# Kernel tuning notes

Measured on AMD Instinct MI355X. Metric: run time of the kernel, lower is better.

Reference implementation:

```python
import jax, jax.numpy as jnp
import numpy as np

M, IN, OUT, R = 8192, 4096, 4096, 16  # tokens, in_features, out_features, lora rank


def setup_inputs() -> dict:
    key = jax.random.key(0)
    k = jax.random.split(key, 7)
    # symmetric int8 quantized activations and weights
    x = jax.random.randint(k[0], (M, IN), -127, 128, dtype=jnp.int8)
    weight = jax.random.randint(k[1], (OUT, IN), -127, 128, dtype=jnp.int8)
    # per-token activation scales and per-output-channel weight scales
    x_scales = jax.random.uniform(k[2], (M,), jnp.float32, 0.5, 1.5) / 127.0
    scales = jax.random.uniform(k[3], (OUT,), jnp.float32, 0.5, 1.5) / 127.0
    bias = jax.random.normal(k[4], (OUT,), jnp.float32)
    # module inits lora_a ~ N(0, 1/r); lora_b is zeros in the module but we use
    # small random values so the LoRA path is numerically exercised
    lora_a = jax.random.normal(k[5], (R, IN), jnp.float32) * (1.0 / R)
    lora_b = jax.random.normal(k[6], (OUT, R), jnp.float32) * 0.02
    return dict(x=x, weight=weight, bias=bias, x_scales=x_scales,
                scales=scales, lora_a=lora_a, lora_b=lora_b, fuse_gelu=1)


def reference(x, weight, bias, x_scales, scales, lora_a, lora_b, fuse_gelu):
    acc = jax.lax.dot_general(x, weight, (((1,), (1,)), ((), ())),
                              preferred_element_type=jnp.int32)
    # dequantize with outer product of per-token and per-channel scales
    main = acc.astype(jnp.float32) * x_scales[:, None] * scales[None, :]
    # LoRA correction on the dequantized activations: (x_deq @ A^T) @ B^T
    x_deq = x.astype(jnp.float32) * x_scales[:, None]          # [M, IN]
    lora = (x_deq @ lora_a.T) @ lora_b.T                        # [M, R] @ [R, OUT]
    out = main + lora + bias[None, :]
    if fuse_gelu:  # static Python flag
        out = jax.nn.gelu(out, approximate=True)  # tanh-approx GELU (CUDA fused path)
    return out
```

## Files before the change

### kernel.cpp

```cpp
#include <hip/hip_runtime.h>

#define M_DIM 8192
#define IN_DIM 4096
#define OUT_DIM 4096

typedef int   v4i  __attribute__((ext_vector_type(4)));
typedef int   v16i __attribute__((ext_vector_type(16)));
typedef short v8s  __attribute__((ext_vector_type(8)));
typedef float v4f  __attribute__((ext_vector_type(4)));
typedef float v16f __attribute__((ext_vector_type(16)));

static __device__ __forceinline__ int pack4(int a, int b, int c, int d) {
    return (a & 255) | ((b & 255) << 8) | ((c & 255) << 16) | ((d & 255) << 24);
}

static __device__ __forceinline__ short f2bf(float f) {
    unsigned u = __float_as_uint(f);
    u = (u + 0x7FFFu + ((u >> 16) & 1u)) >> 16;
    return (short)u;
}

static __device__ __forceinline__ short i2bf(int v) {
    float f = (float)v;
    return (short)(__float_as_uint(f) >> 16);
}

static __device__ __forceinline__ float gelu_tanh(float u) {
    float u2 = u * u;
    float p  = fmaf(u2, 0.0356774081f, 0.7978845608f);
    float v  = u * p;
    float e  = __builtin_amdgcn_exp2f(v * 2.8853900818f);
    return u - u * __builtin_amdgcn_rcpf(e + 1.0f);
}

static __device__ __forceinline__ void async_cp16(const signed char* g, signed char* l) {
    __builtin_amdgcn_global_load_lds((const __attribute__((address_space(1))) void*)g,
                                     (__attribute__((address_space(3))) void*)l, 16, 0, 0);
}


__global__ __launch_bounds__(256) void pack_a_kernel(const float* __restrict__ la,
                                                     short* __restrict__ a16) {
    size_t i = ((size_t)blockIdx.x * 256 + threadIdx.x) * 8;
    const float4* p = (const float4*)(la + i);
    float4 a = p[0], b = p[1];
    v8s o;
    o[0] = f2bf(a.x); o[1] = f2bf(a.y); o[2] = f2bf(a.z); o[3] = f2bf(a.w);
    o[4] = f2bf(b.x); o[5] = f2bf(b.y); o[6] = f2bf(b.z); o[7] = f2bf(b.w);
    *(v8s*)(a16 + i) = o;
}

__global__ __launch_bounds__(256) void pack_w_kernel(const int* __restrict__ w,
                                                     signed char* __restrict__ w8t) {
    const int flat = blockIdx.x * 256 + threadIdx.x;
    const int l  = flat & 63;
    const int gp = (flat >> 6) & 15;
    const int kk = (flat >> 10) & 63;
    const int bn = flat >> 16;
    const int n = bn * 256 + ((gp >> 1) << 5) + (l & 31);
    const int k = kk * 64 + ((gp & 1) << 5) + ((l >> 5) << 4);
    const int4* p = (const int4*)(w + (size_t)n * IN_DIM + k);
    int4 a = p[0], b = p[1], c = p[2], d = p[3];
    int4 o;
    o.x = pack4(a.x, a.y, a.z, a.w);
    o.y = pack4(b.x, b.y, b.z, b.w);
    o.z = pack4(c.x, c.y, c.z, c.w);
    o.w = pack4(d.x, d.y, d.z, d.w);
    *(int4*)(w8t + (size_t)flat * 16) = o;
}

__global__ __launch_bounds__(256) void pack_x_lora_kernel(const int* __restrict__ x,
                                                          const short* __restrict__ a16,
                                                          signed char* __restrict__ x8t,
                                                          float* __restrict__ T) {
    __shared__ float red[4 * 256];
    const int tid = threadIdx.x;
    const int lane = tid & 63, wv = tid >> 6;
    const int fr = lane & 15, fq = lane >> 4;
    const int m0 = blockIdx.x * 16;
    const int bm = m0 >> 8;
    const int g  = (m0 >> 5) & 7;
    const int l5 = (m0 & 16) + fr;
    const int row = m0 + fr;

    v4f acc = {0.f, 0.f, 0.f, 0.f};
#pragma unroll 2
    for (int kt = 0; kt < 32; ++kt) {
        const int k  = wv * 1024 + kt * 32 + fq * 8;
        const int4* xp = (const int4*)(x + (size_t)row * IN_DIM + k);
        int4 a = xp[0], b = xp[1];
        const int kk = k >> 6, c = (k >> 4) & 3, j8 = (k >> 3) & 1;
        int2 pk = make_int2(pack4(a.x, a.y, a.z, a.w), pack4(b.x, b.y, b.z, b.w));
        *(int2*)(x8t + ((size_t)((bm * 64 + kk) * 16 + g * 2 + (c >> 1))) * 1024 +
                 ((c & 1) * 32 + l5) * 16 + j8 * 8) = pk;
        v8s xa;
        xa[0] = i2bf(a.x); xa[1] = i2bf(a.y); xa[2] = i2bf(a.z); xa[3] = i2bf(a.w);
        xa[4] = i2bf(b.x); xa[5] = i2bf(b.y); xa[6] = i2bf(b.z); xa[7] = i2bf(b.w);
        v8s aa = *(const v8s*)(a16 + (size_t)fr * IN_DIM + k);
        acc = __builtin_amdgcn_mfma_f32_16x16x32_bf16(xa, aa, acc, 0, 0, 0);
    }
    *(v4f*)&red[wv * 256 + lane * 4] = acc;
    __syncthreads();

    float s = red[tid] + red[256 + tid] + red[512 + tid] + red[768 + tid];
    const int sl = tid >> 2, j = tid & 3;
    const int r16 = ((sl >> 4) << 2) + j, col = sl & 15;
    T[(size_t)(m0 + r16) * 16 + col] = s;
}

__global__ __launch_bounds__(512, 2) void q8_gemm_kernel(
    const signed char* __restrict__ x8t, const signed char* __restrict__ w8t,
    const float* __restrict__ Tp, const float* __restrict__ lbm,
    const float* __restrict__ bias, const float* __restrict__ xsc,
    const float* __restrict__ wsc, const int* __restrict__ gflag,
    float* __restrict__ out) {
    __shared__ __align__(16) signed char smem[98304];

    const int tid  = threadIdx.x;
    const int lane = tid & 63;
    const int wv   = tid >> 6;
    const int wm   = wv >> 2, wn = wv & 3;
    const int b   = blockIdx.x;
    const int xcd = b & 7, rr = b >> 3;
    const int bm  = xcd * 4 + (rr & 3);
    const int bn  = rr >> 2;

    const int lofs = lane * 16;
    const size_t toff = (size_t)tid * 16;
    const signed char* Asrc = x8t + (size_t)bm * (64 * 16 * 1024);
    const signed char* Bsrc = w8t + (size_t)bn * (64 * 16 * 1024);

    v16i acc[4][2];
    {
        v16i z;
#pragma unroll
        for (int i = 0; i < 16; ++i) z[i] = 0;
#pragma unroll
        for (int mt = 0; mt < 4; ++mt)
#pragma unroll
            for (int nt = 0; nt < 2; ++nt) acc[mt][nt] = z;
    }

#pragma unroll
    for (int tt = 0; tt < 2; ++tt) {
        const signed char* ga = Asrc + (size_t)tt * 16384 + toff;
        const signed char* gb = Bsrc + (size_t)tt * 16384 + toff;
        signed char* l = smem + tt * 32768 + (wv << 10);
        async_cp16(ga,        l);
        async_cp16(ga + 8192, l + 8192);
        async_cp16(gb,        l + 16384);
        async_cp16(gb + 8192, l + 24576);
    }
    asm volatile("s_waitcnt vmcnt(4)" ::: "memory");
    __builtin_amdgcn_s_barrier();

    int cur = 0;
    for (int t = 0; t < 64; ++t) {
        const signed char* Ab = smem + cur * 32768;
        const signed char* Bb = Ab + 16384;
        const int sb = (cur == 0) ? 2 : cur - 1;
        signed char* sl = smem + sb * 32768 + (wv << 10);
        const signed char* ga = Asrc + (size_t)(t + 2) * 16384 + toff;
        const signed char* gb = Bsrc + (size_t)(t + 2) * 16384 + toff;
        const bool pf = (t < 62);

        v4i a0, a1, a2, a3, b0, b1;

        a0 = *(const v4i*)(Ab + (wm * 8 + 0) * 1024 + lofs);
        a1 = *(const v4i*)(Ab + (wm * 8 + 2) * 1024 + lofs);
        b0 = *(const v4i*)(Bb + (wn * 4 + 0) * 1024 + lofs);
        b1 = *(const v4i*)(Bb + (wn * 4 + 2) * 1024 + lofs);
        if (pf) async_cp16(ga, sl);
        __builtin_amdgcn_s_barrier();
        __builtin_amdgcn_s_setprio(1);
        acc[0][0] = __builtin_amdgcn_mfma_i32_32x32x32_i8(a0, b0, acc[0][0], 0, 0, 0);
        acc[0][1] = __builtin_amdgcn_mfma_i32_32x32x32_i8(a0, b1, acc[0][1], 0, 0, 0);
        acc[1][0] = __builtin_amdgcn_mfma_i32_32x32x32_i8(a1, b0, acc[1][0], 0, 0, 0);
        acc[1][1] = __builtin_amdgcn_mfma_i32_32x32x32_i8(a1, b1, acc[1][1], 0, 0, 0);
        __builtin_amdgcn_s_setprio(0);
        __builtin_amdgcn_s_barrier();

        a2 = *(const v4i*)(Ab + (wm * 8 + 4) * 1024 + lofs);
        a3 = *(const v4i*)(Ab + (wm * 8 + 6) * 1024 + lofs);
        if (pf) async_cp16(ga + 8192, sl + 8192);
        __builtin_amdgcn_s_barrier();
        __builtin_amdgcn_s_setprio(1);
        acc[2][0] = __builtin_amdgcn_mfma_i32_32x32x32_i8(a2, b0, acc[2][0], 0, 0, 0);
        acc[2][1] = __builtin_amdgcn_mfma_i32_32x32x32_i8(a2, b1, acc[2][1], 0, 0, 0);
        acc[3][0] = __builtin_amdgcn_mfma_i32_32x32x32_i8(a3, b0, acc[3][0], 0, 0, 0);
        acc[3][1] = __builtin_amdgcn_mfma_i32_32x32x32_i8(a3, b1, acc[3][1], 0, 0, 0);
        __builtin_amdgcn_s_setprio(0);
        __builtin_amdgcn_s_barrier();

        a0 = *(const v4i*)(Ab + (wm * 8 + 1) * 1024 + lofs);
        a1 = *(const v4i*)(Ab + (wm * 8 + 3) * 1024 + lofs);
        b0 = *(const v4i*)(Bb + (wn * 4 + 1) * 1024 + lofs);
        b1 = *(const v4i*)(Bb + (wn * 4 + 3) * 1024 + lofs);
        if (pf) async_cp16(gb, sl + 16384);
        __builtin_amdgcn_s_barrier();
        __builtin_amdgcn_s_setprio(1);
        acc[0][0] = __builtin_amdgcn_mfma_i32_32x32x32_i8(a0, b0, acc[0][0], 0, 0, 0);
        acc[0][1] = __builtin_amdgcn_mfma_i32_32x32x32_i8(a0, b1, acc[0][1], 0, 0, 0);
        acc[1][0] = __builtin_amdgcn_mfma_i32_32x32x32_i8(a1, b0, acc[1][0], 0, 0, 0);
        acc[1][1] = __builtin_amdgcn_mfma_i32_32x32x32_i8(a1, b1, acc[1][1], 0, 0, 0);
        __builtin_amdgcn_s_setprio(0);
        __builtin_amdgcn_s_barrier();

        a2 = *(const v4i*)(Ab + (wm * 8 + 5) * 1024 + lofs);
        a3 = *(const v4i*)(Ab + (wm * 8 + 7) * 1024 + lofs);
        if (pf) async_cp16(gb + 8192, sl + 24576);
        __builtin_amdgcn_s_barrier();
        __builtin_amdgcn_s_setprio(1);
        acc[2][0] = __builtin_amdgcn_mfma_i32_32x32x32_i8(a2, b0, acc[2][0], 0, 0, 0);
        acc[2][1] = __builtin_amdgcn_mfma_i32_32x32x32_i8(a2, b1, acc[2][1], 0, 0, 0);
        acc[3][0] = __builtin_amdgcn_mfma_i32_32x32x32_i8(a3, b0, acc[3][0], 0, 0, 0);
        acc[3][1] = __builtin_amdgcn_mfma_i32_32x32x32_i8(a3, b1, acc[3][1], 0, 0, 0);
        __builtin_amdgcn_s_setprio(0);
        if (pf) {
            asm volatile("s_waitcnt vmcnt(4)" ::: "memory");
        } else if (t == 62) {
            asm volatile("s_waitcnt vmcnt(0)" ::: "memory");
        }
        __builtin_amdgcn_s_barrier();
        cur = (cur == 2) ? 0 : cur + 1;
    }

    const int mbase = bm * 256 + wm * 128;
    const int nbase = bn * 256 + wn * 64;
    const int l31 = lane & 31, lh = lane >> 5;
    const bool dg = (*gflag) != 0;

    v8s tf[4], bf[2];
#pragma unroll
    for (int mt = 0; mt < 4; ++mt) {
        const float* t0 = Tp + (size_t)(mbase + mt * 32 + l31) * 16 + lh * 8;
        v8s v;
#pragma unroll
        for (int j = 0; j < 8; ++j) v[j] = f2bf(t0[j]);
        tf[mt] = v;
    }
#pragma unroll
    for (int nt = 0; nt < 2; ++nt) {
        const float* bp = lbm + (size_t)(nbase + nt * 32 + l31) * 16 + lh * 8;
        v8s v;
#pragma unroll
        for (int j = 0; j < 8; ++j) v[j] = f2bf(bp[j]);
        bf[nt] = v;
    }
    float wsa[2], bba[2];
#pragma unroll
    for (int nt = 0; nt < 2; ++nt) {
        const int col = nbase + nt * 32 + l31;
        wsa[nt] = wsc[col];
        bba[nt] = bias[col];
    }

#pragma unroll
    for (int mt = 0; mt < 4; ++mt) {
        const int rowb = mbase + mt * 32 + lh * 4;
        float4 xs0 = *(const float4*)(xsc + rowb);
        float4 xs1 = *(const float4*)(xsc + rowb + 8);
        float4 xs2 = *(const float4*)(xsc + rowb + 16);
        float4 xs3 = *(const float4*)(xsc + rowb + 24);
        float xsv[16] = {xs0.x, xs0.y, xs0.z, xs0.w, xs1.x, xs1.y, xs1.z, xs1.w,
                         xs2.x, xs2.y, xs2.z, xs2.w, xs3.x, xs3.y, xs3.z, xs3.w};
#pragma unroll
        for (int nt = 0; nt < 2; ++nt) {
            v16f fa;
#pragma unroll
            for (int i = 0; i < 16; ++i) fa[i] = (float)acc[mt][nt][i] * wsa[nt];
            fa = __builtin_amdgcn_mfma_f32_32x32x16_bf16(tf[mt], bf[nt], fa, 0, 0, 0);
            const int col = nbase + nt * 32 + l31;
#pragma unroll
            for (int r = 0; r < 16; ++r) {
                float u = fmaf(xsv[r], fa[r], bba[nt]);
                if (dg) u = gelu_tanh(u);
                out[(size_t)(rowb + (r & 3) + 8 * (r >> 2)) * OUT_DIM + col] = u;
            }
        }
    }
}

extern "C" void kernel_launch(void* const* d_in, const int* in_sizes, int n_in,
                              void* d_out, int out_size, void* d_ws, size_t ws_size,
                              hipStream_t stream) {
    const int*   x     = (const int*)d_in[0];
    const int*   wt    = (const int*)d_in[1];
    const float* bias  = (const float*)d_in[2];
    const float* xsc   = (const float*)d_in[3];
    const float* wsc   = (const float*)d_in[4];
    const float* la    = (const float*)d_in[5];
    const float* lb    = (const float*)d_in[6];
    const int*   gflag = (const int*)d_in[7];
    float* out = (float*)d_out;

    signed char* x8t = (signed char*)d_ws;
    signed char* w8t = x8t + (size_t)M_DIM * IN_DIM;
    float* T = (float*)(w8t + (size_t)OUT_DIM * IN_DIM);
    short* a16 = (short*)w8t;

    pack_a_kernel<<<16 * IN_DIM / (8 * 256), 256, 0, stream>>>(la, a16);
    pack_x_lora_kernel<<<M_DIM / 16, 256, 0, stream>>>(x, a16, x8t, T);
    pack_w_kernel<<<(size_t)OUT_DIM * IN_DIM / (16 * 256), 256, 0, stream>>>(wt, w8t);
    q8_gemm_kernel<<<(M_DIM / 256) * (OUT_DIM / 256), 512, 0, stream>>>(
        x8t, w8t, T, lb, bias, xsc, wsc, gflag, out);
}
```

Before: 436.8 us.

## Shrink GEMM block tile to 256x128 with 4 waves and fewer barriers

Changes the int8 GEMM block tile from 256x256 with 8 waves to 256x128 with 4 waves, doubling the grid and reducing LDS per block from 96KB to 72KB. Each wave still computes a 128x64 output tile, now with a 2x2 wave layout, and B tiles are addressed as halves of the packed 256-column panels. The main loop is restructured from four barrier-separated phases into two, loading all four A fragments at once and issuing three async copies per phase. The goal is higher occupancy and less barrier overhead, at the cost of lower A reuse per block and more global traffic for the A panel.

```diff
diff --git a/kernel.cpp b/kernel.cpp
--- a/kernel.cpp
+++ b/kernel.cpp
@@ -108,18 +108,18 @@
     T[(size_t)(m0 + r16) * 16 + col] = s;
 }
 
-__global__ __launch_bounds__(512, 2) void q8_gemm_kernel(
+__global__ __launch_bounds__(256, 2) void q8_gemm_kernel(
     const signed char* __restrict__ x8t, const signed char* __restrict__ w8t,
     const float* __restrict__ Tp, const float* __restrict__ lbm,
     const float* __restrict__ bias, const float* __restrict__ xsc,
     const float* __restrict__ wsc, const int* __restrict__ gflag,
     float* __restrict__ out) {
-    __shared__ __align__(16) signed char smem[98304];
+    __shared__ __align__(16) signed char smem[73728];
 
     const int tid  = threadIdx.x;
     const int lane = tid & 63;
     const int wv   = tid >> 6;
-    const int wm   = wv >> 2, wn = wv & 3;
+    const int wm   = wv >> 1, wn = wv & 1;
     const int b   = blockIdx.x;
     const int xcd = b & 7, rr = b >> 3;
     const int bm  = xcd * 4 + (rr & 3);
@@ -128,7 +128,7 @@
     const int lofs = lane * 16;
     const size_t toff = (size_t)tid * 16;
     const signed char* Asrc = x8t + (size_t)bm * (64 * 16 * 1024);
-    const signed char* Bsrc = w8t + (size_t)bn * (64 * 16 * 1024);
+    const signed char* Bsrc = w8t + (size_t)(bn >> 1) * (64 * 16 * 1024) + (bn & 1) * 8192;
 
     v16i acc[4][2];
     {
@@ -143,90 +143,90 @@
 
 #pragma unroll
     for (int tt = 0; tt < 2; ++tt) {
-        const signed char* ga = Asrc + (size_t)tt * 16384 + toff;
-        const signed char* gb = Bsrc + (size_t)tt * 16384 + toff;
-        signed char* l = smem + tt * 32768 + (wv << 10);
-        async_cp16(ga,        l);
-        async_cp16(ga + 8192, l + 8192);
-        async_cp16(gb,        l + 16384);
-        async_cp16(gb + 8192, l + 24576);
-    }
-    asm volatile("s_waitcnt vmcnt(4)" ::: "memory");
+        const signed char* gA = Asrc + (size_t)tt * 16384 + toff;
+        const signed char* gB = Bsrc + (size_t)tt * 16384 + toff;
+        signed char* sA = smem + tt * 24576 + (wv << 10);
+        signed char* sB = sA + 16384;
+        async_cp16(gA,         sA);
+        async_cp16(gA + 4096,  sA + 4096);
+        async_cp16(gA + 8192,  sA + 8192);
+        async_cp16(gA + 12288, sA + 12288);
+        async_cp16(gB,         sB);
+        async_cp16(gB + 4096,  sB + 4096);
+    }
+    asm volatile("s_waitcnt vmcnt(6)" ::: "memory");
     __builtin_amdgcn_s_barrier();
 
     int cur = 0;
     for (int t = 0; t < 64; ++t) {
-        const signed char* Ab = smem + cur * 32768;
+        const signed char* Ab = smem + cur * 24576;
         const signed char* Bb = Ab + 16384;
         const int sb = (cur == 0) ? 2 : cur - 1;
-        signed char* sl = smem + sb * 32768 + (wv << 10);
-        const signed char* ga = Asrc + (size_t)(t + 2) * 16384 + toff;
-        const signed char* gb = Bsrc + (size_t)(t + 2) * 16384 + toff;
+        signed char* sA = smem + sb * 24576 + (wv << 10);
+        signed char* sB = sA + 16384;
+        const signed char* gA = Asrc + (size_t)(t + 2) * 16384 + toff;
+        const signed char* gB = Bsrc + (size_t)(t + 2) * 16384 + toff;
         const bool pf = (t < 62);
 
         v4i a0, a1, a2, a3, b0, b1;
 
-        a0 = *(const v4i*)(Ab + (wm * 8 + 0) * 1024 + lofs);
-        a1 = *(const v4i*)(Ab + (wm * 8 + 2) * 1024 + lofs);
-        b0 = *(const v4i*)(Bb + (wn * 4 + 0) * 1024 + lofs);
-        b1 = *(const v4i*)(Bb + (wn * 4 + 2) * 1024 + lofs);
-        if (pf) async_cp16(ga, sl);
+        a0 = *(const v4i*)(Ab + ((wm * 4 + 0) * 2 + 0) * 1024 + lofs);
+        a1 = *(const v4i*)(Ab + ((wm * 4 + 1) * 2 + 0) * 1024 + lofs);
+        a2 = *(const v4i*)(Ab + ((wm * 4 + 2) * 2 + 0) * 1024 + lofs);
+        a3 = *(const v4i*)(Ab + ((wm * 4 + 3) * 2 + 0) * 1024 + lofs);
+        b0 = *(const v4i*)(Bb + ((wn * 2 + 0) * 2 + 0) * 1024 + lofs);
+        b1 = *(const v4i*)(Bb + ((wn * 2 + 1) * 2 + 0) * 1024 + lofs);
+        if (pf) {
+            async_cp16(gA,        sA);
+            async_cp16(gA + 4096, sA + 4096);
+            async_cp16(gB,        sB);
+        }
         __builtin_amdgcn_s_barrier();
         __builtin_amdgcn_s_setprio(1);
         acc[0][0] = __builtin_amdgcn_mfma_i32_32x32x32_i8(a0, b0, acc[0][0], 0, 0, 0);
         acc[0][1] = __builtin_amdgcn_mfma_i32_32x32x32_i8(a0, b1, acc[0][1], 0, 0, 0);
         acc[1][0] = __builtin_amdgcn_mfma_i32_32x32x32_i8(a1, b0, acc[1][0], 0, 0, 0);
         acc[1][1] = __builtin_amdgcn_mfma_i32_32x32x32_i8(a1, b1, acc[1][1], 0, 0, 0);
-        __builtin_amdgcn_s_setprio(0);
-        __builtin_amdgcn_s_barrier();
-
-        a2 = *(const v4i*)(Ab + (wm * 8 + 4) * 1024 + lofs);
-        a3 = *(const v4i*)(Ab + (wm * 8 + 6) * 1024 + lofs);
-        if (pf) async_cp16(ga + 8192, sl + 8192);
-        __builtin_amdgcn_s_barrier();
-        __builtin_amdgcn_s_setprio(1);
         acc[2][0] = __builtin_amdgcn_mfma_i32_32x32x32_i8(a2, b0, acc[2][0], 0, 0, 0);
         acc[2][1] = __builtin_amdgcn_mfma_i32_32x32x32_i8(a2, b1, acc[2][1], 0, 0, 0);
         acc[3][0] = __builtin_amdgcn_mfma_i32_32x32x32_i8(a3, b0, acc[3][0], 0, 0, 0);
         acc[3][1] = __builtin_amdgcn_mfma_i32_32x32x32_i8(a3, b1, acc[3][1], 0, 0, 0);
         __builtin_amdgcn_s_setprio(0);
-        __builtin_amdgcn_s_barrier();
-
-        a0 = *(const v4i*)(Ab + (wm * 8 + 1) * 1024 + lofs);
-        a1 = *(const v4i*)(Ab + (wm * 8 + 3) * 1024 + lofs);
-        b0 = *(const v4i*)(Bb + (wn * 4 + 1) * 1024 + lofs);
-        b1 = *(const v4i*)(Bb + (wn * 4 + 3) * 1024 + lofs);
-        if (pf) async_cp16(gb, sl + 16384);
+
+        a0 = *(const v4i*)(Ab + ((wm * 4 + 0) * 2 + 1) * 1024 + lofs);
+        a1 = *(const v4i*)(Ab + ((wm * 4 + 1) * 2 + 1) * 1024 + lofs);
+        a2 = *(const v4i*)(Ab + ((wm * 4 + 2) * 2 + 1) * 1024 + lofs);
+        a3 = *(const v4i*)(Ab + ((wm * 4 + 3) * 2 + 1) * 1024 + lofs);
+        b0 = *(const v4i*)(Bb + ((wn * 2 + 0) * 2 + 1) * 1024 + lofs);
+        b1 = *(const v4i*)(Bb + ((wn * 2 + 1) * 2 + 1) * 1024 + lofs);
+        if (pf) {
+            async_cp16(gA + 8192,  sA + 8192);
+            async_cp16(gA + 12288, sA + 12288);
+            async_cp16(gB + 4096,  sB + 4096);
+        }
         __builtin_amdgcn_s_barrier();
         __builtin_amdgcn_s_setprio(1);
         acc[0][0] = __builtin_amdgcn_mfma_i32_32x32x32_i8(a0, b0, acc[0][0], 0, 0, 0);
         acc[0][1] = __builtin_amdgcn_mfma_i32_32x32x32_i8(a0, b1, acc[0][1], 0, 0, 0);
         acc[1][0] = __builtin_amdgcn_mfma_i32_32x32x32_i8(a1, b0, acc[1][0], 0, 0, 0);
         acc[1][1] = __builtin_amdgcn_mfma_i32_32x32x32_i8(a1, b1, acc[1][1], 0, 0, 0);
-        __builtin_amdgcn_s_setprio(0);
-        __builtin_amdgcn_s_barrier();
-
-        a2 = *(const v4i*)(Ab + (wm * 8 + 5) * 1024 + lofs);
-        a3 = *(const v4i*)(Ab + (wm * 8 + 7) * 1024 + lofs);
-        if (pf) async_cp16(gb + 8192, sl + 24576);
-        __builtin_amdgcn_s_barrier();
-        __builtin_amdgcn_s_setprio(1);
         acc[2][0] = __builtin_amdgcn_mfma_i32_32x32x32_i8(a2, b0, acc[2][0], 0, 0, 0);
         acc[2][1] = __builtin_amdgcn_mfma_i32_32x32x32_i8(a2, b1, acc[2][1], 0, 0, 0);
         acc[3][0] = __builtin_amdgcn_mfma_i32_32x32x32_i8(a3, b0, acc[3][0], 0, 0, 0);
         acc[3][1] = __builtin_amdgcn_mfma_i32_32x32x32_i8(a3, b1, acc[3][1], 0, 0, 0);
         __builtin_amdgcn_s_setprio(0);
+
         if (pf) {
-            asm volatile("s_waitcnt vmcnt(4)" ::: "memory");
+            asm volatile("s_waitcnt vmcnt(6)" ::: "memory");
         } else if (t == 62) {
             asm volatile("s_waitcnt vmcnt(0)" ::: "memory");
         }
-        __builtin_amdgcn_s_barrier();
+        if (t < 63) __builtin_amdgcn_s_barrier();
         cur = (cur == 2) ? 0 : cur + 1;
     }
 
     const int mbase = bm * 256 + wm * 128;
-    const int nbase = bn * 256 + wn * 64;
+    const int nbase = bn * 128 + wn * 64;
     const int l31 = lane & 31, lh = lane >> 5;
     const bool dg = (*gflag) != 0;
 
@@ -302,6 +302,6 @@
     pack_a_kernel<<<16 * IN_DIM / (8 * 256), 256, 0, stream>>>(la, a16);
     pack_x_lora_kernel<<<M_DIM / 16, 256, 0, stream>>>(x, a16, x8t, T);
     pack_w_kernel<<<(size_t)OUT_DIM * IN_DIM / (16 * 256), 256, 0, stream>>>(wt, w8t);
-    q8_gemm_kernel<<<(M_DIM / 256) * (OUT_DIM / 256), 512, 0, stream>>>(
+    q8_gemm_kernel<<<(M_DIM / 256) * (OUT_DIM / 128), 256, 0, stream>>>(
         x8t, w8t, T, lb, bias, xsc, wsc, gflag, out);
 }
```

Result: no change. 434.4 us (-0.5%).
